# Optimization experiments

Hardware: AMD Instinct MI355X
Metric: run time of the kernel (lower is better)

Reference implementation:

```python
import jax, jax.numpy as jnp
import numpy as np

B, S, I, H = 16, 2048, 1024, 1024

def setup_inputs() -> dict:
    key = jax.random.key(0)
    ks = jax.random.split(key, 6)
    scale_ih = 1.0 / np.sqrt(I)
    scale_hh = 1.0 / np.sqrt(H)
    return {
        "x": jax.random.normal(ks[0], (B, S, I), dtype=jnp.float32),
        "hx": jax.random.normal(ks[1], (B, H), dtype=jnp.float32),
        "W_ih": jax.random.normal(ks[2], (H, I), dtype=jnp.float32) * scale_ih,
        "W_hh": jax.random.normal(ks[3], (H, H), dtype=jnp.float32) * scale_hh,
        "b_ih": jax.random.normal(ks[4], (H,), dtype=jnp.float32) * scale_ih,
        "b_hh": jax.random.normal(ks[5], (H,), dtype=jnp.float32) * scale_hh,
    }

def reference(x, hx, W_ih, W_hh, b_ih, b_hh):
    # Faithful to RecurrentCellWrapper: the Python loop passes the SAME
    # initial hx to the cell at every timestep (hx is never updated),
    # so all steps are independent and fully vectorizable.
    # cell: h' = tanh(x_t @ W_ih^T + b_ih + hx @ W_hh^T + b_hh)
    h_term = hx @ W_hh.T + b_hh + b_ih            # [B, H], shared across steps
    x_term = jnp.einsum('bsi,hi->bsh', x, W_ih)   # [B, S, H]
    out = jnp.tanh(x_term + h_term[:, None, :])   # [B, S, H]
    # batch_first=True: output already [batch, seq, hidden]
    return out
```

## Files before the change

kernel.cpp:

```cpp
#include <hip/hip_runtime.h>
#include <hip/hip_bf16.h>
#include <stdint.h>


#define M_TOT 32768
#define N_TOT 1024
#define K_TOT 1024

typedef short short8 __attribute__((ext_vector_type(8)));
typedef float f32x4  __attribute__((ext_vector_type(4)));

#define WS_WBF_OFF 0
#define WS_HT_OFF  2097152

__device__ __forceinline__ unsigned short f32_to_bf16_rne(float f) {
    union { float f; unsigned int u; } v; v.f = f;
    unsigned int u = v.u;
    unsigned int r = u + 0x7fffu + ((u >> 16) & 1u);
    return (unsigned short)(r >> 16);
}

__device__ __forceinline__ unsigned int cvt_pk_bf16(float lo, float hi) {
    unsigned int r;
    asm("v_cvt_pk_bf16_f32 %0, %1, %2" : "=v"(r) : "v"(lo), "v"(hi));
    return r;
}

__device__ __forceinline__ float fast_tanh(float z) {
    float e = __expf(2.0f * z);
    return 1.0f - 2.0f / (e + 1.0f);
}

__global__ void prep_kernel(const float* __restrict__ hx,
                            const float* __restrict__ whh,
                            const float* __restrict__ bih,
                            const float* __restrict__ bhh,
                            const float* __restrict__ wih,
                            float* __restrict__ ht,
                            unsigned short* __restrict__ wbf) {
    if (blockIdx.x < 4096) {
        int lane = threadIdx.x & 63;
        int w    = threadIdx.x >> 6;
        int wg   = blockIdx.x * 4 + w;
        int b = wg >> 10, h = wg & 1023;
        const float* hr = hx  + (long long)b * 1024;
        const float* wr = whh + (long long)h * 1024;
        float s = 0.f;
#pragma unroll
        for (int p = 0; p < 4; ++p) {
            int idx = p * 256 + lane * 4;
            float4 a = *(const float4*)(hr + idx);
            float4 c = *(const float4*)(wr + idx);
            s += a.x * c.x + a.y * c.y + a.z * c.z + a.w * c.w;
        }
#pragma unroll
        for (int d = 32; d > 0; d >>= 1) s += __shfl_down(s, d, 64);
        if (lane == 0) ht[wg] = s + bih[h] + bhh[h];
    } else {
        int g = (blockIdx.x - 4096) * 256 + threadIdx.x;
        for (int v = g; v < 131072; v += 32768) {
            long long base = (long long)v * 8;
            float4 a = *(const float4*)(wih + base);
            float4 b = *(const float4*)(wih + base + 4);
            union { unsigned short s[8]; uint4 u; } o;
            o.s[0] = f32_to_bf16_rne(a.x); o.s[1] = f32_to_bf16_rne(a.y);
            o.s[2] = f32_to_bf16_rne(a.z); o.s[3] = f32_to_bf16_rne(a.w);
            o.s[4] = f32_to_bf16_rne(b.x); o.s[5] = f32_to_bf16_rne(b.y);
            o.s[6] = f32_to_bf16_rne(b.z); o.s[7] = f32_to_bf16_rne(b.w);
            *(uint4*)(wbf + base) = o.u;
        }
    }
}

#define GLDS16(gp, lp) \
    __builtin_amdgcn_global_load_lds((const __attribute__((address_space(1))) void*)(gp), \
                                     (__attribute__((address_space(3))) void*)(lp), 16, 0, 0)

__global__ __launch_bounds__(256) void gemm_tanh_kernel(
    const float* __restrict__ X,
    const unsigned short* __restrict__ Bm,
    const float* __restrict__ ht,
    float* __restrict__ out)
{
    __shared__ __align__(16) char lds[16384];

    const int tid = threadIdx.x;
    const int w = tid >> 6, l = tid & 63;

    const int bid  = blockIdx.x;
    const int widx = (bid & 7) * 256 + (bid >> 3);
    const int tile_m = widx >> 3;
    const int tile_n = widx & 7;
    const int m0 = tile_m << 7, n0 = tile_n << 7;

    const int rowA  = tid >> 1;
    const int halfA = tid & 1;
    const float* gA = X + (long long)(m0 + rowA) * K_TOT + halfA * 16;
    const int swzA = (rowA >> 1) & 3;
    char* lA0 = lds + rowA * 64 + (((halfA * 2 + 0 + swzA) & 3) << 4);
    char* lA1 = lds + rowA * 64 + (((halfA * 2 + 1 + swzA) & 3) << 4);

    const int r0 = (w * 2 + 0) * 16 + (l >> 2);
    const int r1 = (w * 2 + 1) * 16 + (l >> 2);
    const int slot = l & 3;
    const int qg0 = (slot - (r0 >> 1)) & 3;
    const int qg1 = (slot - (r1 >> 1)) & 3;
    const unsigned short* gB0 = Bm + (long long)(n0 + r0) * K_TOT + qg0 * 8;
    const unsigned short* gB1 = Bm + (long long)(n0 + r1) * K_TOT + qg1 * 8;
    char* ldsB0 = lds + 8192 + (w * 2 + 0) * 1024;
    char* ldsB1 = lds + 8192 + (w * 2 + 1) * 1024;

    const int wm = w & 1, wn = w >> 1;
    const int lm = l & 15, q = l >> 4;
    int offA[4], offB[4];
#pragma unroll
    for (int t = 0; t < 4; ++t) {
        int rr = wm * 64 + t * 16 + lm;
        offA[t] = rr * 64 + (((q + (rr >> 1)) & 3) << 4);
        int nn = wn * 64 + t * 16 + lm;
        offB[t] = 8192 + nn * 64 + (((q + (nn >> 1)) & 3) << 4);
    }

    f32x4 acc[4][4];
#pragma unroll
    for (int i = 0; i < 4; ++i)
#pragma unroll
        for (int j = 0; j < 4; ++j)
            acc[i][j] = (f32x4){0.f, 0.f, 0.f, 0.f};

    float4 a0 = *(const float4*)(gA + 0);
    float4 a1 = *(const float4*)(gA + 4);
    float4 a2 = *(const float4*)(gA + 8);
    float4 a3 = *(const float4*)(gA + 12);

    for (int k0 = 0; k0 < K_TOT; k0 += 32) {
        uint4 pk0, pk1;
        pk0.x = cvt_pk_bf16(a0.x, a0.y); pk0.y = cvt_pk_bf16(a0.z, a0.w);
        pk0.z = cvt_pk_bf16(a1.x, a1.y); pk0.w = cvt_pk_bf16(a1.z, a1.w);
        pk1.x = cvt_pk_bf16(a2.x, a2.y); pk1.y = cvt_pk_bf16(a2.z, a2.w);
        pk1.z = cvt_pk_bf16(a3.x, a3.y); pk1.w = cvt_pk_bf16(a3.z, a3.w);
        *(uint4*)lA0 = pk0;
        *(uint4*)lA1 = pk1;
        GLDS16(gB0 + k0, ldsB0);
        GLDS16(gB1 + k0, ldsB1);
        __syncthreads();

        short8 af[4], bf[4];
#pragma unroll
        for (int t = 0; t < 4; ++t) {
            af[t] = *(const short8*)(lds + offA[t]);
            bf[t] = *(const short8*)(lds + offB[t]);
        }

        if (k0 + 32 < K_TOT) {
            const float* nA = gA + k0 + 32;
            a0 = *(const float4*)(nA + 0);
            a1 = *(const float4*)(nA + 4);
            a2 = *(const float4*)(nA + 8);
            a3 = *(const float4*)(nA + 12);
        }

#pragma unroll
        for (int mt = 0; mt < 4; ++mt)
#pragma unroll
            for (int nt = 0; nt < 4; ++nt)
                acc[mt][nt] = __builtin_amdgcn_mfma_f32_16x16x32_bf16(
                    af[mt], bf[nt], acc[mt][nt], 0, 0, 0);
        __syncthreads();
    }

    const int b = tile_m >> 4;
    float htv[4];
#pragma unroll
    for (int nt = 0; nt < 4; ++nt)
        htv[nt] = ht[b * 1024 + n0 + wn * 64 + nt * 16 + lm];

#pragma unroll
    for (int mt = 0; mt < 4; ++mt) {
#pragma unroll
        for (int nt = 0; nt < 4; ++nt) {
            int n = n0 + wn * 64 + nt * 16 + lm;
#pragma unroll
            for (int r = 0; r < 4; ++r) {
                int m = m0 + wm * 64 + mt * 16 + q * 4 + r;
                float z = acc[mt][nt][r] + htv[nt];
                out[(long long)m * N_TOT + n] = fast_tanh(z);
            }
        }
    }
}

extern "C" void kernel_launch(void* const* d_in, const int* in_sizes, int n_in,
                              void* d_out, int out_size, void* d_ws, size_t ws_size,
                              hipStream_t stream) {
    const float* x    = (const float*)d_in[0];
    const float* hx   = (const float*)d_in[1];
    const float* wih  = (const float*)d_in[2];
    const float* whh  = (const float*)d_in[3];
    const float* bih  = (const float*)d_in[4];
    const float* bhh  = (const float*)d_in[5];
    float* out = (float*)d_out;

    unsigned short* wbf = (unsigned short*)((char*)d_ws + WS_WBF_OFF);
    float*          htp = (float*)((char*)d_ws + WS_HT_OFF);

    prep_kernel<<<4224, 256, 0, stream>>>(hx, whh, bih, bhh, wih, htp, wbf);
    gemm_tanh_kernel<<<2048, 256, 0, stream>>>(x, wbf, htp, out);
}
```

Before: 371.4 us.

## Double-buffer LDS and software-pipeline A/B loads in GEMM-tanh kernel

Switches the GEMM main loop to a two-stage LDS double buffer. B tiles for step t+1 are issued via global_load_lds and A registers for step t+2 are prefetched, all while MFMAs run on the current buffer. Manual s_waitcnt and a single s_barrier per iteration replace the two __syncthreads. This doubles LDS use to 32KB, which may lower occupancy, and it depends on hand-placed vmcnt counts being correct. Wrap-around indexing issues redundant loads in the last iterations.

```diff
diff --git a/kernel.cpp b/kernel.cpp
--- a/kernel.cpp
+++ b/kernel.cpp
@@ -76,13 +76,60 @@
     __builtin_amdgcn_global_load_lds((const __attribute__((address_space(1))) void*)(gp), \
                                      (__attribute__((address_space(3))) void*)(lp), 16, 0, 0)
 
+#define KITER(T, P, CUR0, CUR1, CUR2, CUR3, NXT0, NXT1, NXT2, NXT3)            \
+  {                                                                            \
+              \
+    const int kb = (((T) + 1) & 31) * 32;                                      \
+    GLDS16(gB0 + kb, ldsB0 + ((P) ^ 1) * 16384);                               \
+    GLDS16(gB1 + kb, ldsB1 + ((P) ^ 1) * 16384);                               \
+    __builtin_amdgcn_sched_barrier(0);         \
+                     \
+    const int ka = (((T) + 2) & 31) * 32;                                      \
+    NXT0 = *(const float4*)(gA + ka + 0);                                      \
+    NXT1 = *(const float4*)(gA + ka + 4);                                      \
+    NXT2 = *(const float4*)(gA + ka + 8);                                      \
+    NXT3 = *(const float4*)(gA + ka + 12);                                     \
+                                       \
+    {                                                                          \
+      const char* lb = lds + (P) * 16384;                                      \
+      short8 af[4], bfr[4];                                                    \
+      _Pragma("unroll")                                                        \
+      for (int t4 = 0; t4 < 4; ++t4) {                                         \
+        af[t4]  = *(const short8*)(lb + offA[t4]);                             \
+        bfr[t4] = *(const short8*)(lb + offB[t4]);                             \
+      }                                                                        \
+      _Pragma("unroll")                                                        \
+      for (int mt = 0; mt < 4; ++mt)                                           \
+        _Pragma("unroll")                                                      \
+        for (int nt = 0; nt < 4; ++nt)                                         \
+          acc[mt][nt] = __builtin_amdgcn_mfma_f32_16x16x32_bf16(               \
+              af[mt], bfr[nt], acc[mt][nt], 0, 0, 0);                          \
+    }                                                                          \
+         \
+    {                                                                          \
+      uint4 pk0, pk1;                                                          \
+      pk0.x = cvt_pk_bf16(CUR0.x, CUR0.y); pk0.y = cvt_pk_bf16(CUR0.z, CUR0.w);\
+      pk0.z = cvt_pk_bf16(CUR1.x, CUR1.y); pk0.w = cvt_pk_bf16(CUR1.z, CUR1.w);\
+      pk1.x = cvt_pk_bf16(CUR2.x, CUR2.y); pk1.y = cvt_pk_bf16(CUR2.z, CUR2.w);\
+      pk1.z = cvt_pk_bf16(CUR3.x, CUR3.y); pk1.w = cvt_pk_bf16(CUR3.z, CUR3.w);\
+      *(uint4*)(lA0 + ((P) ^ 1) * 16384) = pk0;                                \
+      *(uint4*)(lA1 + ((P) ^ 1) * 16384) = pk1;                                \
+    }                                                                          \
+                     \
+    __builtin_amdgcn_sched_barrier(0);                                         \
+    asm volatile("s_waitcnt vmcnt(4)" ::: "memory");                           \
+    asm volatile("s_waitcnt lgkmcnt(0)" ::: "memory");                         \
+    __builtin_amdgcn_s_barrier();                                              \
+    __builtin_amdgcn_sched_barrier(0);                                         \
+  }
+
 __global__ __launch_bounds__(256) void gemm_tanh_kernel(
     const float* __restrict__ X,
     const unsigned short* __restrict__ Bm,
     const float* __restrict__ ht,
     float* __restrict__ out)
 {
-    __shared__ __align__(16) char lds[16384];
+    __shared__ __align__(16) char lds[32768];
 
     const int tid = threadIdx.x;
     const int w = tid >> 6, l = tid & 63;
@@ -128,46 +175,40 @@
         for (int j = 0; j < 4; ++j)
             acc[i][j] = (f32x4){0.f, 0.f, 0.f, 0.f};
 
-    float4 a0 = *(const float4*)(gA + 0);
-    float4 a1 = *(const float4*)(gA + 4);
-    float4 a2 = *(const float4*)(gA + 8);
-    float4 a3 = *(const float4*)(gA + 12);
-
-    for (int k0 = 0; k0 < K_TOT; k0 += 32) {
+    float4 s0_0, s0_1, s0_2, s0_3;
+    float4 s1_0, s1_1, s1_2, s1_3;
+
+    s0_0 = *(const float4*)(gA + 0);
+    s0_1 = *(const float4*)(gA + 4);
+    s0_2 = *(const float4*)(gA + 8);
+    s0_3 = *(const float4*)(gA + 12);
+    GLDS16(gB0, ldsB0);
+    GLDS16(gB1, ldsB1);
+    __builtin_amdgcn_sched_barrier(0);
+    {
         uint4 pk0, pk1;
-        pk0.x = cvt_pk_bf16(a0.x, a0.y); pk0.y = cvt_pk_bf16(a0.z, a0.w);
-        pk0.z = cvt_pk_bf16(a1.x, a1.y); pk0.w = cvt_pk_bf16(a1.z, a1.w);
-        pk1.x = cvt_pk_bf16(a2.x, a2.y); pk1.y = cvt_pk_bf16(a2.z, a2.w);
-        pk1.z = cvt_pk_bf16(a3.x, a3.y); pk1.w = cvt_pk_bf16(a3.z, a3.w);
+        pk0.x = cvt_pk_bf16(s0_0.x, s0_0.y); pk0.y = cvt_pk_bf16(s0_0.z, s0_0.w);
+        pk0.z = cvt_pk_bf16(s0_1.x, s0_1.y); pk0.w = cvt_pk_bf16(s0_1.z, s0_1.w);
+        pk1.x = cvt_pk_bf16(s0_2.x, s0_2.y); pk1.y = cvt_pk_bf16(s0_2.z, s0_2.w);
+        pk1.z = cvt_pk_bf16(s0_3.x, s0_3.y); pk1.w = cvt_pk_bf16(s0_3.z, s0_3.w);
         *(uint4*)lA0 = pk0;
         *(uint4*)lA1 = pk1;
-        GLDS16(gB0 + k0, ldsB0);
-        GLDS16(gB1 + k0, ldsB1);
-        __syncthreads();
-
-        short8 af[4], bf[4];
-#pragma unroll
-        for (int t = 0; t < 4; ++t) {
-            af[t] = *(const short8*)(lds + offA[t]);
-            bf[t] = *(const short8*)(lds + offB[t]);
-        }
-
-        if (k0 + 32 < K_TOT) {
-            const float* nA = gA + k0 + 32;
-            a0 = *(const float4*)(nA + 0);
-            a1 = *(const float4*)(nA + 4);
-            a2 = *(const float4*)(nA + 8);
-            a3 = *(const float4*)(nA + 12);
-        }
-
-#pragma unroll
-        for (int mt = 0; mt < 4; ++mt)
-#pragma unroll
-            for (int nt = 0; nt < 4; ++nt)
-                acc[mt][nt] = __builtin_amdgcn_mfma_f32_16x16x32_bf16(
-                    af[mt], bf[nt], acc[mt][nt], 0, 0, 0);
-        __syncthreads();
-    }
+    }
+    s1_0 = *(const float4*)(gA + 32 + 0);
+    s1_1 = *(const float4*)(gA + 32 + 4);
+    s1_2 = *(const float4*)(gA + 32 + 8);
+    s1_3 = *(const float4*)(gA + 32 + 12);
+    __builtin_amdgcn_sched_barrier(0);
+    asm volatile("s_waitcnt vmcnt(4)" ::: "memory");
+    asm volatile("s_waitcnt lgkmcnt(0)" ::: "memory");
+    __builtin_amdgcn_s_barrier();
+    __builtin_amdgcn_sched_barrier(0);
+
+    for (int tt = 0; tt < 32; tt += 2) {
+        KITER(tt,     0, s1_0, s1_1, s1_2, s1_3, s0_0, s0_1, s0_2, s0_3);
+        KITER(tt + 1, 1, s0_0, s0_1, s0_2, s0_3, s1_0, s1_1, s1_2, s1_3);
+    }
+    asm volatile("s_waitcnt vmcnt(0)" ::: "memory");
 
     const int b = tile_m >> 4;
     float htv[4];
```

New measurement: 361.7 us. -2.6%, faster.

## Double-buffer GEMM LDS and stream fp32 A tiles directly via global_load_lds

Applied to the files above, without the earlier changes.

The GEMM main loop moves to a two-stage LDS ping-pong with a single barrier per K step. Both the fp32 activation tile and the bf16 weight tile are prefetched asynchronously into the next buffer with global_load_lds. The fp32-to-bf16 conversion of A now happens after reading from LDS instead of before storing to it. This removes register staging and one barrier per iteration, but raises LDS use to 48KB per block, requests three blocks per CU through launch bounds, and doubles LDS read traffic for A.

```diff
diff --git a/kernel.cpp b/kernel.cpp
--- a/kernel.cpp
+++ b/kernel.cpp
@@ -76,13 +76,51 @@
     __builtin_amdgcn_global_load_lds((const __attribute__((address_space(1))) void*)(gp), \
                                      (__attribute__((address_space(3))) void*)(lp), 16, 0, 0)
 
-__global__ __launch_bounds__(256) void gemm_tanh_kernel(
+#define KITER(KNEXT, P, STAGE)                                                 \
+  {                                                                            \
+    if (STAGE) {                                                               \
+      _Pragma("unroll")                                                        \
+      for (int j = 0; j < 4; ++j)                                              \
+        GLDS16(gA[j] + (KNEXT), lA[j] + ((P) ^ 1) * 24576);                    \
+      GLDS16(gB0 + (KNEXT), lB0 + ((P) ^ 1) * 24576);                          \
+      GLDS16(gB1 + (KNEXT), lB1 + ((P) ^ 1) * 24576);                          \
+    }                                                                          \
+    {                                                                          \
+      const char* lb = lds + (P) * 24576;                                      \
+      f32x4 alo[4], ahi[4]; short8 bfr[4];                                     \
+      _Pragma("unroll")                                                        \
+      for (int t4 = 0; t4 < 4; ++t4) {                                         \
+        alo[t4] = *(const f32x4*)(lb + offA0[t4]);                             \
+        ahi[t4] = *(const f32x4*)(lb + offA1[t4]);                             \
+        bfr[t4] = *(const short8*)(lb + offB[t4]);                             \
+      }                                                                        \
+      short8 af[4];                                                            \
+      _Pragma("unroll")                                                        \
+      for (int t4 = 0; t4 < 4; ++t4) {                                         \
+        union { uint4 u; short8 s; } cv;                                       \
+        cv.u.x = cvt_pk_bf16(alo[t4].x, alo[t4].y);                            \
+        cv.u.y = cvt_pk_bf16(alo[t4].z, alo[t4].w);                            \
+        cv.u.z = cvt_pk_bf16(ahi[t4].x, ahi[t4].y);                            \
+        cv.u.w = cvt_pk_bf16(ahi[t4].z, ahi[t4].w);                            \
+        af[t4] = cv.s;                                                         \
+      }                                                                        \
+      _Pragma("unroll")                                                        \
+      for (int mt = 0; mt < 4; ++mt)                                           \
+        _Pragma("unroll")                                                      \
+        for (int nt = 0; nt < 4; ++nt)                                         \
+          acc[mt][nt] = __builtin_amdgcn_mfma_f32_16x16x32_bf16(               \
+              af[mt], bfr[nt], acc[mt][nt], 0, 0, 0);                          \
+    }                                                                          \
+    __syncthreads();                                                           \
+  }
+
+__global__ __launch_bounds__(256, 3) void gemm_tanh_kernel(
     const float* __restrict__ X,
     const unsigned short* __restrict__ Bm,
     const float* __restrict__ ht,
     float* __restrict__ out)
 {
-    __shared__ __align__(16) char lds[16384];
+    __shared__ __align__(16) char lds[49152];
 
     const int tid = threadIdx.x;
     const int w = tid >> 6, l = tid & 63;
@@ -93,12 +131,16 @@
     const int tile_n = widx & 7;
     const int m0 = tile_m << 7, n0 = tile_n << 7;
 
-    const int rowA  = tid >> 1;
-    const int halfA = tid & 1;
-    const float* gA = X + (long long)(m0 + rowA) * K_TOT + halfA * 16;
-    const int swzA = (rowA >> 1) & 3;
-    char* lA0 = lds + rowA * 64 + (((halfA * 2 + 0 + swzA) & 3) << 4);
-    char* lA1 = lds + rowA * 64 + (((halfA * 2 + 1 + swzA) & 3) << 4);
+    const float* gA[4];
+    char* lA[4];
+#pragma unroll
+    for (int j = 0; j < 4; ++j) {
+        int R  = (w * 4 + j) * 16 + (l >> 2);
+        int kh = R >> 7, r = R & 127;
+        int qg = ((l & 3) - (r >> 1)) & 3;
+        gA[j] = X + (long long)(m0 + r) * K_TOT + kh * 16 + qg * 4;
+        lA[j] = lds + (w * 4 + j) * 1024;
+    }
 
     const int r0 = (w * 2 + 0) * 16 + (l >> 2);
     const int r1 = (w * 2 + 1) * 16 + (l >> 2);
@@ -107,18 +149,21 @@
     const int qg1 = (slot - (r1 >> 1)) & 3;
     const unsigned short* gB0 = Bm + (long long)(n0 + r0) * K_TOT + qg0 * 8;
     const unsigned short* gB1 = Bm + (long long)(n0 + r1) * K_TOT + qg1 * 8;
-    char* ldsB0 = lds + 8192 + (w * 2 + 0) * 1024;
-    char* ldsB1 = lds + 8192 + (w * 2 + 1) * 1024;
+    char* lB0 = lds + 16384 + (w * 2 + 0) * 1024;
+    char* lB1 = lds + 16384 + (w * 2 + 1) * 1024;
 
     const int wm = w & 1, wn = w >> 1;
     const int lm = l & 15, q = l >> 4;
-    int offA[4], offB[4];
+    int offA0[4], offA1[4], offB[4];
 #pragma unroll
     for (int t = 0; t < 4; ++t) {
         int rr = wm * 64 + t * 16 + lm;
-        offA[t] = rr * 64 + (((q + (rr >> 1)) & 3) << 4);
+        int abase = (q >> 1) * 8192 + rr * 64;
+        int c0 = 2 * (q & 1);
+        offA0[t] = abase + (((c0 + 0 + (rr >> 1)) & 3) << 4);
+        offA1[t] = abase + (((c0 + 1 + (rr >> 1)) & 3) << 4);
         int nn = wn * 64 + t * 16 + lm;
-        offB[t] = 8192 + nn * 64 + (((q + (nn >> 1)) & 3) << 4);
+        offB[t] = 16384 + nn * 64 + (((q + (nn >> 1)) & 3) << 4);
     }
 
     f32x4 acc[4][4];
@@ -128,46 +173,18 @@
         for (int j = 0; j < 4; ++j)
             acc[i][j] = (f32x4){0.f, 0.f, 0.f, 0.f};
 
-    float4 a0 = *(const float4*)(gA + 0);
-    float4 a1 = *(const float4*)(gA + 4);
-    float4 a2 = *(const float4*)(gA + 8);
-    float4 a3 = *(const float4*)(gA + 12);
-
-    for (int k0 = 0; k0 < K_TOT; k0 += 32) {
-        uint4 pk0, pk1;
-        pk0.x = cvt_pk_bf16(a0.x, a0.y); pk0.y = cvt_pk_bf16(a0.z, a0.w);
-        pk0.z = cvt_pk_bf16(a1.x, a1.y); pk0.w = cvt_pk_bf16(a1.z, a1.w);
-        pk1.x = cvt_pk_bf16(a2.x, a2.y); pk1.y = cvt_pk_bf16(a2.z, a2.w);
-        pk1.z = cvt_pk_bf16(a3.x, a3.y); pk1.w = cvt_pk_bf16(a3.z, a3.w);
-        *(uint4*)lA0 = pk0;
-        *(uint4*)lA1 = pk1;
-        GLDS16(gB0 + k0, ldsB0);
-        GLDS16(gB1 + k0, ldsB1);
-        __syncthreads();
-
-        short8 af[4], bf[4];
-#pragma unroll
-        for (int t = 0; t < 4; ++t) {
-            af[t] = *(const short8*)(lds + offA[t]);
-            bf[t] = *(const short8*)(lds + offB[t]);
-        }
-
-        if (k0 + 32 < K_TOT) {
-            const float* nA = gA + k0 + 32;
-            a0 = *(const float4*)(nA + 0);
-            a1 = *(const float4*)(nA + 4);
-            a2 = *(const float4*)(nA + 8);
-            a3 = *(const float4*)(nA + 12);
-        }
-
-#pragma unroll
-        for (int mt = 0; mt < 4; ++mt)
-#pragma unroll
-            for (int nt = 0; nt < 4; ++nt)
-                acc[mt][nt] = __builtin_amdgcn_mfma_f32_16x16x32_bf16(
-                    af[mt], bf[nt], acc[mt][nt], 0, 0, 0);
-        __syncthreads();
-    }
+#pragma unroll
+    for (int j = 0; j < 4; ++j) GLDS16(gA[j], lA[j]);
+    GLDS16(gB0, lB0);
+    GLDS16(gB1, lB1);
+    __syncthreads();
+
+    for (int i = 0; i < 30; i += 2) {
+        KITER((i + 1) * 32, 0, true);
+        KITER((i + 2) * 32, 1, true);
+    }
+    KITER(31 * 32, 0, true);
+    KITER(0,       1, false);
 
     const int b = tile_m >> 4;
     float htv[4];
```

Result: faster. 350.4 us (-5.7%).
